# Kernel optimization log

Measured on AMD Instinct MI355X. Metric: run time of the kernel, lower is better.

## Reference

```python
import jax, jax.numpy as jnp
import numpy as np

D_MODEL = 1024
NUM_HEADS = 16
D_K = D_MODEL // NUM_HEADS  # 64
B, T = 2, 2048


def rope_tables(seq_len, d_k):
    # Matches RotaryPositionalEmbedding + the slice apply_rotary takes:
    # only cos/sin of freqs (dim d_k//2) are used.
    half = d_k // 2
    inv_freq = 1.0 / (10000.0 ** (jnp.arange(0, d_k, 2, dtype=jnp.float32) / d_k))  # (half,)
    t = jnp.arange(seq_len, dtype=jnp.float32)
    freqs = jnp.einsum('i,j->ij', t, inv_freq)  # (T, half)
    return jnp.cos(freqs), jnp.sin(freqs)


def apply_rotary(x, cos, sin):
    # x: (B, H, T, D); rotate first 2*half dims as two halves
    half = x.shape[-1] // 2
    x1, x2 = x[..., :half], x[..., half:2 * half]
    c = cos[None, None, :x.shape[2], :half]
    s = sin[None, None, :x.shape[2], :half]
    return jnp.concatenate([x1 * c - x2 * s, x1 * s + x2 * c], axis=-1)


def setup_inputs() -> dict:
    key = jax.random.key(0)
    ks = jax.random.split(key, 5)
    scale = 1.0 / np.sqrt(D_MODEL)
    return {
        'x': jax.random.normal(ks[0], (B, T, D_MODEL), dtype=jnp.float32),
        'wq': jax.random.normal(ks[1], (D_MODEL, D_MODEL), dtype=jnp.float32) * scale,
        'wk': jax.random.normal(ks[2], (D_MODEL, D_MODEL), dtype=jnp.float32) * scale,
        'wv': jax.random.normal(ks[3], (D_MODEL, D_MODEL), dtype=jnp.float32) * scale,
        'wo': jax.random.normal(ks[4], (D_MODEL, D_MODEL), dtype=jnp.float32) * scale,
    }


def reference(x, wq, wk, wv, wo):
    Bs, Ts, _ = x.shape
    def proj(w):
        # nn.Linear: x @ w.T, then split heads -> (B, H, T, d_k)
        return (x @ w.T).reshape(Bs, Ts, NUM_HEADS, D_K).transpose(0, 2, 1, 3)
    Q, K, V = proj(wq), proj(wk), proj(wv)
    cos, sin = rope_tables(Ts, D_K)
    Q = apply_rotary(Q, cos, sin)
    K = apply_rotary(K, cos, sin)
    scores = jnp.einsum('bhqd,bhkd->bhqk', Q, K) / jnp.sqrt(jnp.float32(D_K))
    attn = jax.nn.softmax(scores, axis=-1)  # dropout is identity in eval
    out = jnp.einsum('bhqk,bhkd->bhqd', attn, V)
    out = out.transpose(0, 2, 1, 3).reshape(Bs, Ts, D_MODEL)
    return out @ wo.T
```

## Files before the change

### kernel.cpp

```cpp
#include <hip/hip_runtime.h>
#include <math.h>

typedef __attribute__((ext_vector_type(8))) short short8;
typedef __attribute__((ext_vector_type(4))) short short4v;
typedef __attribute__((ext_vector_type(4))) float f32x4;
typedef __attribute__((ext_vector_type(16))) float f32x16;

#define D_MODEL 1024
#define NUM_HEADS 16
#define D_K 64
#define B_SZ 2
#define T_SZ 2048
#define M_ROWS (B_SZ * T_SZ)
#define LSTR 72
#define LOG2E 1.4426950408889634f
#define KVSPLIT 1024

__device__ __forceinline__ unsigned short f2bf(float f) {
    union { float f; unsigned int u; } v; v.f = f;
    unsigned int r = v.u + 0x7FFF + ((v.u >> 16) & 1);
    return (unsigned short)(r >> 16);
}
__device__ __forceinline__ void gload_lds16(const void* g, void* l) {
    __builtin_amdgcn_global_load_lds(
        (const __attribute__((address_space(1))) unsigned int*)g,
        (__attribute__((address_space(3))) unsigned int*)l, 16, 0, 0);
}
__device__ __forceinline__ int cvtpk(float lo, float hi) {
    int r;
    asm("v_cvt_pk_bf16_f32 %0, %1, %2" : "=v"(r) : "v"(lo), "v"(hi));
    return r;
}
__device__ __forceinline__ float fast_exp2(float x) {
#if __has_builtin(__builtin_amdgcn_exp2f)
    return __builtin_amdgcn_exp2f(x);
#else
    float r; asm("v_exp_f32 %0, %1" : "=v"(r) : "v"(x)); return r;
#endif
}

__global__ __launch_bounds__(256) void prep_all(
    const float* __restrict__ x,  const float* __restrict__ w0,
    const float* __restrict__ w1, const float* __restrict__ w2,
    const float* __restrict__ w3, unsigned short* __restrict__ dst,
    float2* __restrict__ tab)
{
    const size_t NX8 = (size_t)M_ROWS * D_MODEL / 8;
    const size_t NW8 = (size_t)D_MODEL * D_MODEL / 8;
    if (blockIdx.x >= 4096) {
        int idx = (blockIdx.x - 4096) * 256 + threadIdx.x;
        int t = idx >> 5, i = idx & 31;
        const float invf = (float)pow(10000.0, -(double)i / 32.0);
        float s, c;
        sincosf((float)t * invf, &s, &c);
        tab[idx] = make_float2(c, s);
        return;
    }
    size_t i = (size_t)blockIdx.x * 256 + threadIdx.x;
    const float* src; size_t off;
    if (i < NX8) { src = x; off = i; }
    else {
        size_t j = i - NX8;
        int ws = (int)(j >> 17);
        off = j & (NW8 - 1);
        src = (ws == 0) ? w0 : (ws == 1) ? w1 : (ws == 2) ? w2 : w3;
    }
    const float4* p = (const float4*)src + 2 * off;
    float4 a = p[0], b = p[1];
    short8 o;
    o[0] = f2bf(a.x); o[1] = f2bf(a.y); o[2] = f2bf(a.z); o[3] = f2bf(a.w);
    o[4] = f2bf(b.x); o[5] = f2bf(b.y); o[6] = f2bf(b.z); o[7] = f2bf(b.w);
    *((short8*)dst + i) = o;
}

__global__ __launch_bounds__(256) void gemm_qkv(
    const unsigned short* __restrict__ Xb,
    const unsigned short* __restrict__ Wb,
    unsigned short* __restrict__ Qb,
    unsigned short* __restrict__ Kb,
    unsigned short* __restrict__ Vtg,
    const float2* __restrict__ tab)
{
    __shared__ unsigned short Als[128 * 64];
    __shared__ unsigned short Bls[128 * 64];

    const int tid = threadIdx.x;
    const int lane = tid & 63, wid = tid >> 6;
    const int g = lane >> 4, c16 = lane & 15;
    const int wr = wid >> 1, wc = wid & 1;

    const int bid = blockIdx.x;
    const int xcd = bid & 7, slot = bid >> 3;
    const int bm = (xcd & 3) * 8 + (slot & 7);
    const int bn = (xcd >> 2) * 12 + (slot >> 3);
    const int m0 = bm * 128, n0p = bn * 128;
    const int z = n0p >> 10, n0c = n0p & 1023;

    const int l8 = lane >> 3, l7 = lane & 7;
    const int scol = 8 * (l7 ^ l8);
    const unsigned short* xsrc = Xb + (size_t)(m0 + wid * 32 + l8) * D_MODEL + scol;
    const unsigned short* wsrc = Wb + (size_t)(n0p + wid * 32 + l8) * D_MODEL + scol;

    f32x4 acc[4][4] = {};

    for (int k0 = 0; k0 < D_MODEL; k0 += 64) {
        __syncthreads();
#pragma unroll
        for (int i = 0; i < 4; i++) {
            gload_lds16(xsrc + (size_t)i * 8 * D_MODEL + k0, Als + (wid * 32 + i * 8) * 64);
            gload_lds16(wsrc + (size_t)i * 8 * D_MODEL + k0, Bls + (wid * 32 + i * 8) * 64);
        }
        __syncthreads();
#pragma unroll
        for (int kk = 0; kk < 64; kk += 32) {
            short8 af[4], bf[4];
            const int sw = (c16 & 7) * 8;
#pragma unroll
            for (int mf = 0; mf < 4; mf++)
                af[mf] = *(const short8*)&Als[(wr * 64 + mf * 16 + c16) * 64 +
                                              ((kk + g * 8) ^ sw)];
#pragma unroll
            for (int nf = 0; nf < 4; nf++)
                bf[nf] = *(const short8*)&Bls[(wc * 64 + nf * 16 + c16) * 64 +
                                              ((kk + g * 8) ^ sw)];
#pragma unroll
            for (int mf = 0; mf < 4; mf++)
#pragma unroll
                for (int nf = 0; nf < 4; nf++)
                    acc[mf][nf] = __builtin_amdgcn_mfma_f32_16x16x32_bf16(
                        af[mf], bf[nf], acc[mf][nf], 0, 0, 0);
        }
    }

    if (z < 2) {
        const float qs = (z == 0) ? 0.125f * LOG2E : 1.0f;
        unsigned short* Y = (z == 0) ? Qb : Kb;
#pragma unroll
        for (int mf = 0; mf < 4; mf++)
#pragma unroll
            for (int j = 0; j < 4; j++) {
                int row = m0 + wr * 64 + mf * 16 + g * 4 + j;
                int t = row & (T_SZ - 1);
#pragma unroll
                for (int nf = 0; nf < 2; nf++) {
                    float2 cs = tab[t * 32 + nf * 16 + c16];
                    float a = acc[mf][nf][j], b2 = acc[mf][nf + 2][j];
                    acc[mf][nf][j]     = (a * cs.x - b2 * cs.y) * qs;
                    acc[mf][nf + 2][j] = (a * cs.y + b2 * cs.x) * qs;
                }
            }
#pragma unroll
        for (int mf = 0; mf < 4; mf++)
#pragma unroll
            for (int nf = 0; nf < 4; nf++)
#pragma unroll
                for (int j = 0; j < 4; j++) {
                    int row = m0 + wr * 64 + mf * 16 + g * 4 + j;
                    int col = n0c + wc * 64 + nf * 16 + c16;
                    Y[(size_t)row * D_MODEL + col] = f2bf(acc[mf][nf][j]);
                }
    } else {
#pragma unroll
        for (int mf = 0; mf < 4; mf++) {
            int row0 = m0 + wr * 64 + mf * 16 + g * 4;
            int bq = row0 >> 11;
            int t0 = row0 & (T_SZ - 1);
#pragma unroll
            for (int nf = 0; nf < 4; nf++) {
                int col = n0c + wc * 64 + nf * 16 + c16;
                int h = col >> 6, d = col & 63;
                short4v pk;
#pragma unroll
                for (int j = 0; j < 4; j++) pk[j] = (short)f2bf(acc[mf][nf][j]);
                *(short4v*)&Vtg[(size_t)((bq * 16 + h) * 64 + d) * T_SZ + t0] = pk;
            }
        }
    }
}

__global__ __launch_bounds__(256) void gemm_out(
    const unsigned short* __restrict__ Xb,
    const unsigned short* __restrict__ W,
    float* __restrict__ Y)
{
    __shared__ unsigned short Als[128 * 64];
    __shared__ unsigned short Bls[64 * 64];

    const int tid = threadIdx.x;
    const int lane = tid & 63, wid = tid >> 6;
    const int g = lane >> 4, c16 = lane & 15;
    const int wr = wid >> 1, wc = wid & 1;

    const int bid = blockIdx.x;
    const int xcd = bid & 7, slot = bid >> 3;
    const int bm = (xcd & 3) * 8 + (slot & 7);
    const int bn = (xcd >> 2) * 8 + (slot >> 3);
    const int m0 = bm * 128, n0 = bn * 64;

    const int l8 = lane >> 3, l7 = lane & 7;
    const int scol = 8 * (l7 ^ l8);
    const unsigned short* xsrc = Xb + (size_t)(m0 + wid * 32 + l8) * D_MODEL + scol;
    const unsigned short* wsrc = W + (size_t)(n0 + wid * 16 + l8) * D_MODEL + scol;

    f32x4 acc[4][2] = {};

    for (int k0 = 0; k0 < D_MODEL; k0 += 64) {
        __syncthreads();
#pragma unroll
        for (int i = 0; i < 4; i++)
            gload_lds16(xsrc + (size_t)i * 8 * D_MODEL + k0, Als + (wid * 32 + i * 8) * 64);
#pragma unroll
        for (int j = 0; j < 2; j++)
            gload_lds16(wsrc + (size_t)j * 8 * D_MODEL + k0, Bls + (wid * 16 + j * 8) * 64);
        __syncthreads();
#pragma unroll
        for (int kk = 0; kk < 64; kk += 32) {
            short8 af[4], bf[2];
            const int sw = (c16 & 7) * 8;
#pragma unroll
            for (int mf = 0; mf < 4; mf++)
                af[mf] = *(const short8*)&Als[(wr * 64 + mf * 16 + c16) * 64 +
                                              ((kk + g * 8) ^ sw)];
#pragma unroll
            for (int nf = 0; nf < 2; nf++)
                bf[nf] = *(const short8*)&Bls[(wc * 32 + nf * 16 + c16) * 64 +
                                              ((kk + g * 8) ^ sw)];
#pragma unroll
            for (int mf = 0; mf < 4; mf++)
#pragma unroll
                for (int nf = 0; nf < 2; nf++)
                    acc[mf][nf] = __builtin_amdgcn_mfma_f32_16x16x32_bf16(
                        af[mf], bf[nf], acc[mf][nf], 0, 0, 0);
        }
    }

#pragma unroll
    for (int mf = 0; mf < 4; mf++)
#pragma unroll
        for (int nf = 0; nf < 2; nf++)
#pragma unroll
            for (int j = 0; j < 4; j++) {
                int row = m0 + wr * 64 + mf * 16 + g * 4 + j;
                int col = n0 + wc * 32 + nf * 16 + c16;
                Y[(size_t)row * D_MODEL + col] = acc[mf][nf][j];
            }
}

#define PVAL(i) ((i) < 16 ? s0[(i) & 15] : s1[(i) & 15])

__global__ __launch_bounds__(512, 4) void attn_mfma32(
    const unsigned short* __restrict__ Qb,
    const unsigned short* __restrict__ Kb,
    const unsigned short* __restrict__ Vtg,
    unsigned short* __restrict__ Ob)
{
    __shared__ __align__(16) char smem[36864];

    const int tid = threadIdx.x;
    const int lane = tid & 63, wid = tid >> 6;
    const int kz = wid >> 2, wq = wid & 3;
    const int q32 = lane & 31, hi = lane >> 5;

    const int raw = blockIdx.x;
    const int xcd = raw & 7, slot = raw >> 3;
    const int bh = xcd * 4 + (slot >> 4);
    const int qblk = slot & 15;
    const int b = bh >> 4, h = bh & (NUM_HEADS - 1);
    const int q0 = qblk * 128 + wq * 32;

    unsigned short* Ks = (unsigned short*)(smem + kz * 18432);
    unsigned short* Vt = Ks + 64 * LSTR;

    short8 qf[4];
    {
        const unsigned short* qsrc =
            Qb + (size_t)(b * T_SZ + q0 + q32) * D_MODEL + h * D_K + 8 * hi;
#pragma unroll
        for (int s = 0; s < 4; s++) qf[s] = *(const short8*)(qsrc + 16 * s);
    }

    f32x16 oacc0 = {}, oacc1 = {};
    float l = 0.f;

    const int t256 = tid & 255;
    const int krow = t256 >> 2, kcb = t256 & 3;
    const unsigned short* kbase =
        Kb + (size_t)(b * T_SZ + kz * KVSPLIT) * D_MODEL + h * D_K;
    const unsigned short* vtbase =
        Vtg + (size_t)((b * 16 + h) * 64) * T_SZ + kz * KVSPLIT;

    short8 pk0, pk1, pv0, pv1;
#define LOAD_KV(KT) do { \
    const unsigned short* _s = kbase + (size_t)((KT) + krow) * D_MODEL + kcb * 16; \
    pk0 = *(const short8*)_s; pk1 = *(const short8*)(_s + 8); \
    const unsigned short* _v = vtbase + (size_t)krow * T_SZ + (KT) + kcb * 16; \
    pv0 = *(const short8*)_v; pv1 = *(const short8*)(_v + 8); \
  } while (0)

    LOAD_KV(0);

    for (int kt = 0; kt < KVSPLIT; kt += 64) {
        __builtin_amdgcn_sched_barrier(0);
        __builtin_amdgcn_s_barrier();
        __builtin_amdgcn_sched_barrier(0);
        *(short8*)&Ks[krow * LSTR + kcb * 16] = pk0;
        *(short8*)&Ks[krow * LSTR + kcb * 16 + 8] = pk1;
        *(short8*)&Vt[krow * LSTR + kcb * 16] = pv0;
        *(short8*)&Vt[krow * LSTR + kcb * 16 + 8] = pv1;
        if (kt + 64 < KVSPLIT) LOAD_KV(kt + 64);
        asm volatile("s_waitcnt lgkmcnt(0)" ::: "memory");
        __builtin_amdgcn_s_barrier();
        __builtin_amdgcn_sched_barrier(0);

        f32x16 s0 = {}, s1 = {};
        __builtin_amdgcn_s_setprio(1);
#pragma unroll
        for (int s = 0; s < 4; s++) {
            short8 ak0 = *(const short8*)&Ks[q32 * LSTR + 16 * s + 8 * hi];
            short8 ak1 = *(const short8*)&Ks[(32 + q32) * LSTR + 16 * s + 8 * hi];
            s0 = __builtin_amdgcn_mfma_f32_32x32x16_bf16(ak0, qf[s], s0, 0, 0, 0);
            s1 = __builtin_amdgcn_mfma_f32_32x32x16_bf16(ak1, qf[s], s1, 0, 0, 0);
        }
        __builtin_amdgcn_s_setprio(0);

        float ps = 0.f;
#pragma unroll
        for (int r = 0; r < 16; r++) s0[r] = fast_exp2(s0[r]);
#pragma unroll
        for (int r = 0; r < 16; r++) s1[r] = fast_exp2(s1[r]);
#pragma unroll
        for (int r = 0; r < 16; r++) ps += s0[r] + s1[r];
        l += ps;

        __builtin_amdgcn_s_setprio(1);
#pragma unroll
        for (int t = 0; t < 4; t++) {
            const int b0 = 4 * ((2 * t + 0) & 3) + 16 * (t >> 1);
            const int b1 = 4 * ((2 * t + 1) & 3) + 16 * (t >> 1);
            int X0 = cvtpk(PVAL(b0), PVAL(b0 + 1));
            int X1 = cvtpk(PVAL(b0 + 2), PVAL(b0 + 3));
            int Y0 = cvtpk(PVAL(b1), PVAL(b1 + 1));
            int Y1 = cvtpk(PVAL(b1 + 2), PVAL(b1 + 3));
            asm("v_permlane32_swap_b32 %0, %1" : "+v"(X0), "+v"(Y0));
            asm("v_permlane32_swap_b32 %0, %1" : "+v"(X1), "+v"(Y1));
            union { int w[4]; short8 v; } af;
            af.w[0] = X0; af.w[1] = X1; af.w[2] = Y0; af.w[3] = Y1;
            short8 bv0 = *(const short8*)&Vt[q32 * LSTR + 16 * t + 8 * hi];
            short8 bv1 = *(const short8*)&Vt[(32 + q32) * LSTR + 16 * t + 8 * hi];
            oacc0 = __builtin_amdgcn_mfma_f32_32x32x16_bf16(af.v, bv0, oacc0, 0, 0, 0);
            oacc1 = __builtin_amdgcn_mfma_f32_32x32x16_bf16(af.v, bv1, oacc1, 0, 0, 0);
        }
        __builtin_amdgcn_s_setprio(0);
    }

    l += __shfl_xor(l, 32);

    __syncthreads();
    float* cmbO = (float*)smem;
    float* lb   = (float*)(smem + 32768);
    if (kz == 1) {
        if (hi == 0) lb[wq * 32 + q32] = l;
#pragma unroll
        for (int r = 0; r < 16; r++) {
            int qr = (r & 3) + 8 * (r >> 2) + 4 * hi;
            cmbO[wq * 2048 + qr * 64 + q32]      = oacc0[r];
            cmbO[wq * 2048 + qr * 64 + 32 + q32] = oacc1[r];
        }
    }
    __syncthreads();
    if (kz == 0) {
        float linv = 1.f / (l + lb[wq * 32 + q32]);
#pragma unroll
        for (int r = 0; r < 16; r++) {
            int qr = (r & 3) + 8 * (r >> 2) + 4 * hi;
            float iv = __shfl(linv, qr);
            float o0 = (oacc0[r] + cmbO[wq * 2048 + qr * 64 + q32]) * iv;
            float o1 = (oacc1[r] + cmbO[wq * 2048 + qr * 64 + 32 + q32]) * iv;
            size_t row = (size_t)(b * T_SZ + q0 + qr);
            Ob[row * D_MODEL + h * D_K + q32]      = f2bf(o0);
            Ob[row * D_MODEL + h * D_K + 32 + q32] = f2bf(o1);
        }
    }
}

extern "C" void kernel_launch(void* const* d_in, const int* in_sizes, int n_in,
                              void* d_out, int out_size, void* d_ws, size_t ws_size,
                              hipStream_t stream)
{
    const float* x  = (const float*)d_in[0];
    const float* wq = (const float*)d_in[1];
    const float* wk = (const float*)d_in[2];
    const float* wv = (const float*)d_in[3];
    const float* wo = (const float*)d_in[4];
    float* out = (float*)d_out;

    const size_t NX = (size_t)M_ROWS * D_MODEL;
    const size_t NW = (size_t)D_MODEL * D_MODEL;
    unsigned short* xb  = (unsigned short*)d_ws;
    unsigned short* wqb = xb + NX;
    unsigned short* wkb = wqb + NW;
    unsigned short* wvb = wkb + NW;
    unsigned short* wob = wvb + NW;
    unsigned short* Qb  = wob + NW;
    unsigned short* Kb  = Qb + NX;
    unsigned short* Vtg = Kb + NX;
    unsigned short* Ob  = Vtg + NX;
    float2* tab = (float2*)(Ob + NX);

    prep_all<<<dim3(4096 + 256), dim3(256), 0, stream>>>(x, wq, wk, wv, wo, xb, tab);

    gemm_qkv<<<dim3(768), dim3(256), 0, stream>>>(xb, wqb, Qb, Kb, Vtg, tab);

    attn_mfma32<<<dim3(512), dim3(512), 0, stream>>>(Qb, Kb, Vtg, Ob);

    gemm_out<<<dim3(512), dim3(256), 0, stream>>>(Ob, wob, out);
}
```

Measured before the change: 180.6 us.

## Double query rows per attention wave, double-buffer KV LDS, widen out-proj tiles

Each attention wave now processes 64 query rows (two 32-row groups) against each K/V tile, so every LDS K/V fragment load feeds twice as many MFMAs, and the grid is halved to 256 blocks. The K/V shared buffers are double-buffered, which removes one barrier per iteration but doubles LDS use and lowers occupancy to 2 blocks/CU. The output projection GEMM switches to 128x128 tiles with 256 blocks, raising per-block reuse at the cost of more registers and fewer blocks to fill the CUs.

```diff
diff --git a/kernel.cpp b/kernel.cpp
--- a/kernel.cpp
+++ b/kernel.cpp
@@ -184,7 +184,7 @@
     float* __restrict__ Y)
 {
     __shared__ unsigned short Als[128 * 64];
-    __shared__ unsigned short Bls[64 * 64];
+    __shared__ unsigned short Bls[128 * 64];
 
     const int tid = threadIdx.x;
     const int lane = tid & 63, wid = tid >> 6;
@@ -194,41 +194,40 @@
     const int bid = blockIdx.x;
     const int xcd = bid & 7, slot = bid >> 3;
     const int bm = (xcd & 3) * 8 + (slot & 7);
-    const int bn = (xcd >> 2) * 8 + (slot >> 3);
-    const int m0 = bm * 128, n0 = bn * 64;
+    const int bn = (xcd >> 2) * 4 + (slot >> 3);
+    const int m0 = bm * 128, n0 = bn * 128;
 
     const int l8 = lane >> 3, l7 = lane & 7;
     const int scol = 8 * (l7 ^ l8);
     const unsigned short* xsrc = Xb + (size_t)(m0 + wid * 32 + l8) * D_MODEL + scol;
-    const unsigned short* wsrc = W + (size_t)(n0 + wid * 16 + l8) * D_MODEL + scol;
-
-    f32x4 acc[4][2] = {};
+    const unsigned short* wsrc = W + (size_t)(n0 + wid * 32 + l8) * D_MODEL + scol;
+
+    f32x4 acc[4][4] = {};
 
     for (int k0 = 0; k0 < D_MODEL; k0 += 64) {
         __syncthreads();
 #pragma unroll
-        for (int i = 0; i < 4; i++)
+        for (int i = 0; i < 4; i++) {
             gload_lds16(xsrc + (size_t)i * 8 * D_MODEL + k0, Als + (wid * 32 + i * 8) * 64);
-#pragma unroll
-        for (int j = 0; j < 2; j++)
-            gload_lds16(wsrc + (size_t)j * 8 * D_MODEL + k0, Bls + (wid * 16 + j * 8) * 64);
+            gload_lds16(wsrc + (size_t)i * 8 * D_MODEL + k0, Bls + (wid * 32 + i * 8) * 64);
+        }
         __syncthreads();
 #pragma unroll
         for (int kk = 0; kk < 64; kk += 32) {
-            short8 af[4], bf[2];
+            short8 af[4], bf[4];
             const int sw = (c16 & 7) * 8;
 #pragma unroll
             for (int mf = 0; mf < 4; mf++)
                 af[mf] = *(const short8*)&Als[(wr * 64 + mf * 16 + c16) * 64 +
                                               ((kk + g * 8) ^ sw)];
 #pragma unroll
-            for (int nf = 0; nf < 2; nf++)
-                bf[nf] = *(const short8*)&Bls[(wc * 32 + nf * 16 + c16) * 64 +
+            for (int nf = 0; nf < 4; nf++)
+                bf[nf] = *(const short8*)&Bls[(wc * 64 + nf * 16 + c16) * 64 +
                                               ((kk + g * 8) ^ sw)];
 #pragma unroll
             for (int mf = 0; mf < 4; mf++)
 #pragma unroll
-                for (int nf = 0; nf < 2; nf++)
+                for (int nf = 0; nf < 4; nf++)
                     acc[mf][nf] = __builtin_amdgcn_mfma_f32_16x16x32_bf16(
                         af[mf], bf[nf], acc[mf][nf], 0, 0, 0);
         }
@@ -237,24 +236,34 @@
 #pragma unroll
     for (int mf = 0; mf < 4; mf++)
 #pragma unroll
-        for (int nf = 0; nf < 2; nf++)
+        for (int nf = 0; nf < 4; nf++)
 #pragma unroll
             for (int j = 0; j < 4; j++) {
                 int row = m0 + wr * 64 + mf * 16 + g * 4 + j;
-                int col = n0 + wc * 32 + nf * 16 + c16;
+                int col = n0 + wc * 64 + nf * 16 + c16;
                 Y[(size_t)row * D_MODEL + col] = acc[mf][nf][j];
             }
 }
 
-#define PVAL(i) ((i) < 16 ? s0[(i) & 15] : s1[(i) & 15])
-
-__global__ __launch_bounds__(512, 4) void attn_mfma32(
+#define PVX(S0, S1, i) ((i) < 16 ? S0[(i) & 15] : S1[(i) & 15])
+#define MKPF(AF, S0, S1) { \
+    const int b0 = 4 * ((2 * t + 0) & 3) + 16 * (t >> 1); \
+    const int b1 = 4 * ((2 * t + 1) & 3) + 16 * (t >> 1); \
+    int X0 = cvtpk(PVX(S0, S1, b0),     PVX(S0, S1, b0 + 1)); \
+    int X1 = cvtpk(PVX(S0, S1, b0 + 2), PVX(S0, S1, b0 + 3)); \
+    int Y0 = cvtpk(PVX(S0, S1, b1),     PVX(S0, S1, b1 + 1)); \
+    int Y1 = cvtpk(PVX(S0, S1, b1 + 2), PVX(S0, S1, b1 + 3)); \
+    asm("v_permlane32_swap_b32 %0, %1" : "+v"(X0), "+v"(Y0)); \
+    asm("v_permlane32_swap_b32 %0, %1" : "+v"(X1), "+v"(Y1)); \
+    AF.w[0] = X0; AF.w[1] = X1; AF.w[2] = Y0; AF.w[3] = Y1; }
+
+__global__ __launch_bounds__(512, 2) void attn_mfma32(
     const unsigned short* __restrict__ Qb,
     const unsigned short* __restrict__ Kb,
     const unsigned short* __restrict__ Vtg,
     unsigned short* __restrict__ Ob)
 {
-    __shared__ __align__(16) char smem[36864];
+    __shared__ __align__(16) char smem[73728];
 
     const int tid = threadIdx.x;
     const int lane = tid & 63, wid = tid >> 6;
@@ -263,24 +272,25 @@
 
     const int raw = blockIdx.x;
     const int xcd = raw & 7, slot = raw >> 3;
-    const int bh = xcd * 4 + (slot >> 4);
-    const int qblk = slot & 15;
+    const int bh = xcd * 4 + (slot >> 3);
+    const int qblk = slot & 7;
     const int b = bh >> 4, h = bh & (NUM_HEADS - 1);
-    const int q0 = qblk * 128 + wq * 32;
-
-    unsigned short* Ks = (unsigned short*)(smem + kz * 18432);
-    unsigned short* Vt = Ks + 64 * LSTR;
-
-    short8 qf[4];
+    const int qA0 = qblk * 256 + wq * 64;
+
+    short8 qfA[4], qfB[4];
     {
-        const unsigned short* qsrc =
-            Qb + (size_t)(b * T_SZ + q0 + q32) * D_MODEL + h * D_K + 8 * hi;
-#pragma unroll
-        for (int s = 0; s < 4; s++) qf[s] = *(const short8*)(qsrc + 16 * s);
-    }
-
-    f32x16 oacc0 = {}, oacc1 = {};
-    float l = 0.f;
+        const unsigned short* qa =
+            Qb + (size_t)(b * T_SZ + qA0 + q32) * D_MODEL + h * D_K + 8 * hi;
+        const unsigned short* qb2 = qa + (size_t)32 * D_MODEL;
+#pragma unroll
+        for (int s = 0; s < 4; s++) {
+            qfA[s] = *(const short8*)(qa + 16 * s);
+            qfB[s] = *(const short8*)(qb2 + 16 * s);
+        }
+    }
+
+    f32x16 oA0 = {}, oA1 = {}, oB0 = {}, oB1 = {};
+    float lA = 0.f, lB = 0.f;
 
     const int t256 = tid & 255;
     const int krow = t256 >> 2, kcb = t256 & 3;
@@ -299,10 +309,10 @@
 
     LOAD_KV(0);
 
+    int c = 0;
     for (int kt = 0; kt < KVSPLIT; kt += 64) {
-        __builtin_amdgcn_sched_barrier(0);
-        __builtin_amdgcn_s_barrier();
-        __builtin_amdgcn_sched_barrier(0);
+        unsigned short* Ks = (unsigned short*)(smem + kz * 36864 + c * 18432);
+        unsigned short* Vt = Ks + 4608;
         *(short8*)&Ks[krow * LSTR + kcb * 16] = pk0;
         *(short8*)&Ks[krow * LSTR + kcb * 16 + 8] = pk1;
         *(short8*)&Vt[krow * LSTR + kcb * 16] = pv0;
@@ -312,73 +322,85 @@
         __builtin_amdgcn_s_barrier();
         __builtin_amdgcn_sched_barrier(0);
 
-        f32x16 s0 = {}, s1 = {};
+        f32x16 sA0 = {}, sA1 = {}, sB0 = {}, sB1 = {};
         __builtin_amdgcn_s_setprio(1);
 #pragma unroll
         for (int s = 0; s < 4; s++) {
             short8 ak0 = *(const short8*)&Ks[q32 * LSTR + 16 * s + 8 * hi];
             short8 ak1 = *(const short8*)&Ks[(32 + q32) * LSTR + 16 * s + 8 * hi];
-            s0 = __builtin_amdgcn_mfma_f32_32x32x16_bf16(ak0, qf[s], s0, 0, 0, 0);
-            s1 = __builtin_amdgcn_mfma_f32_32x32x16_bf16(ak1, qf[s], s1, 0, 0, 0);
+            sA0 = __builtin_amdgcn_mfma_f32_32x32x16_bf16(ak0, qfA[s], sA0, 0, 0, 0);
+            sB0 = __builtin_amdgcn_mfma_f32_32x32x16_bf16(ak0, qfB[s], sB0, 0, 0, 0);
+            sA1 = __builtin_amdgcn_mfma_f32_32x32x16_bf16(ak1, qfA[s], sA1, 0, 0, 0);
+            sB1 = __builtin_amdgcn_mfma_f32_32x32x16_bf16(ak1, qfB[s], sB1, 0, 0, 0);
         }
         __builtin_amdgcn_s_setprio(0);
 
-        float ps = 0.f;
-#pragma unroll
-        for (int r = 0; r < 16; r++) s0[r] = fast_exp2(s0[r]);
-#pragma unroll
-        for (int r = 0; r < 16; r++) s1[r] = fast_exp2(s1[r]);
-#pragma unroll
-        for (int r = 0; r < 16; r++) ps += s0[r] + s1[r];
-        l += ps;
+        float psA = 0.f, psB = 0.f;
+#pragma unroll
+        for (int r = 0; r < 16; r++) sA0[r] = fast_exp2(sA0[r]);
+#pragma unroll
+        for (int r = 0; r < 16; r++) sA1[r] = fast_exp2(sA1[r]);
+#pragma unroll
+        for (int r = 0; r < 16; r++) sB0[r] = fast_exp2(sB0[r]);
+#pragma unroll
+        for (int r = 0; r < 16; r++) sB1[r] = fast_exp2(sB1[r]);
+#pragma unroll
+        for (int r = 0; r < 16; r++) { psA += sA0[r] + sA1[r]; psB += sB0[r] + sB1[r]; }
+        lA += psA; lB += psB;
 
         __builtin_amdgcn_s_setprio(1);
 #pragma unroll
         for (int t = 0; t < 4; t++) {
-            const int b0 = 4 * ((2 * t + 0) & 3) + 16 * (t >> 1);
-            const int b1 = 4 * ((2 * t + 1) & 3) + 16 * (t >> 1);
-            int X0 = cvtpk(PVAL(b0), PVAL(b0 + 1));
-            int X1 = cvtpk(PVAL(b0 + 2), PVAL(b0 + 3));
-            int Y0 = cvtpk(PVAL(b1), PVAL(b1 + 1));
-            int Y1 = cvtpk(PVAL(b1 + 2), PVAL(b1 + 3));
-            asm("v_permlane32_swap_b32 %0, %1" : "+v"(X0), "+v"(Y0));
-            asm("v_permlane32_swap_b32 %0, %1" : "+v"(X1), "+v"(Y1));
-            union { int w[4]; short8 v; } af;
-            af.w[0] = X0; af.w[1] = X1; af.w[2] = Y0; af.w[3] = Y1;
+            union { int w[4]; short8 v; } pA, pB;
+            MKPF(pA, sA0, sA1);
+            MKPF(pB, sB0, sB1);
             short8 bv0 = *(const short8*)&Vt[q32 * LSTR + 16 * t + 8 * hi];
             short8 bv1 = *(const short8*)&Vt[(32 + q32) * LSTR + 16 * t + 8 * hi];
-            oacc0 = __builtin_amdgcn_mfma_f32_32x32x16_bf16(af.v, bv0, oacc0, 0, 0, 0);
-            oacc1 = __builtin_amdgcn_mfma_f32_32x32x16_bf16(af.v, bv1, oacc1, 0, 0, 0);
+            oA0 = __builtin_amdgcn_mfma_f32_32x32x16_bf16(pA.v, bv0, oA0, 0, 0, 0);
+            oA1 = __builtin_amdgcn_mfma_f32_32x32x16_bf16(pA.v, bv1, oA1, 0, 0, 0);
+            oB0 = __builtin_amdgcn_mfma_f32_32x32x16_bf16(pB.v, bv0, oB0, 0, 0, 0);
+            oB1 = __builtin_amdgcn_mfma_f32_32x32x16_bf16(pB.v, bv1, oB1, 0, 0, 0);
         }
         __builtin_amdgcn_s_setprio(0);
-    }
-
-    l += __shfl_xor(l, 32);
+        c ^= 1;
+    }
+
+    lA += __shfl_xor(lA, 32);
+    lB += __shfl_xor(lB, 32);
 
     __syncthreads();
     float* cmbO = (float*)smem;
-    float* lb   = (float*)(smem + 32768);
+    float* lb   = (float*)(smem + 65536);
     if (kz == 1) {
-        if (hi == 0) lb[wq * 32 + q32] = l;
+        if (hi == 0) { lb[wq * 64 + q32] = lA; lb[wq * 64 + 32 + q32] = lB; }
 #pragma unroll
         for (int r = 0; r < 16; r++) {
             int qr = (r & 3) + 8 * (r >> 2) + 4 * hi;
-            cmbO[wq * 2048 + qr * 64 + q32]      = oacc0[r];
-            cmbO[wq * 2048 + qr * 64 + 32 + q32] = oacc1[r];
+            cmbO[wq * 4096 + qr * 64 + q32]             = oA0[r];
+            cmbO[wq * 4096 + qr * 64 + 32 + q32]        = oA1[r];
+            cmbO[wq * 4096 + (32 + qr) * 64 + q32]      = oB0[r];
+            cmbO[wq * 4096 + (32 + qr) * 64 + 32 + q32] = oB1[r];
         }
     }
     __syncthreads();
     if (kz == 0) {
-        float linv = 1.f / (l + lb[wq * 32 + q32]);
+        float lvA = 1.f / (lA + lb[wq * 64 + q32]);
+        float lvB = 1.f / (lB + lb[wq * 64 + 32 + q32]);
 #pragma unroll
         for (int r = 0; r < 16; r++) {
             int qr = (r & 3) + 8 * (r >> 2) + 4 * hi;
-            float iv = __shfl(linv, qr);
-            float o0 = (oacc0[r] + cmbO[wq * 2048 + qr * 64 + q32]) * iv;
-            float o1 = (oacc1[r] + cmbO[wq * 2048 + qr * 64 + 32 + q32]) * iv;
-            size_t row = (size_t)(b * T_SZ + q0 + qr);
-            Ob[row * D_MODEL + h * D_K + q32]      = f2bf(o0);
-            Ob[row * D_MODEL + h * D_K + 32 + q32] = f2bf(o1);
+            float ivA = __shfl(lvA, qr);
+            float ivB = __shfl(lvB, qr);
+            size_t rowA = (size_t)(b * T_SZ + qA0 + qr);
+            size_t rowB = rowA + 32;
+            Ob[rowA * D_MODEL + h * D_K + q32] =
+                f2bf((oA0[r] + cmbO[wq * 4096 + qr * 64 + q32]) * ivA);
+            Ob[rowA * D_MODEL + h * D_K + 32 + q32] =
+                f2bf((oA1[r] + cmbO[wq * 4096 + qr * 64 + 32 + q32]) * ivA);
+            Ob[rowB * D_MODEL + h * D_K + q32] =
+                f2bf((oB0[r] + cmbO[wq * 4096 + (32 + qr) * 64 + q32]) * ivB);
+            Ob[rowB * D_MODEL + h * D_K + 32 + q32] =
+                f2bf((oB1[r] + cmbO[wq * 4096 + (32 + qr) * 64 + 32 + q32]) * ivB);
         }
     }
 }
@@ -411,7 +433,7 @@
 
     gemm_qkv<<<dim3(768), dim3(256), 0, stream>>>(xb, wqb, Qb, Kb, Vtg, tab);
 
-    attn_mfma32<<<dim3(512), dim3(512), 0, stream>>>(Qb, Kb, Vtg, Ob);
-
-    gemm_out<<<dim3(512), dim3(256), 0, stream>>>(Ob, wob, out);
-}
+    attn_mfma32<<<dim3(256), dim3(512), 0, stream>>>(Qb, Kb, Vtg, Ob);
+
+    gemm_out<<<dim3(256), dim3(256), 0, stream>>>(Ob, wob, out);
+}
```

Measured after the change: 180.7 us. About the same (+0.1%).
